# Kernel tuning notes

Measured on AMD Instinct MI355X. Metric: run time of the kernel, lower is better.

The kernel has to match this reference:

```python
import jax, jax.numpy as jnp
import numpy as np

NUM_EXPERTS = 64
TOP_K = 8
LOAD_EMA_DECAY = 0.999
BIAS_TEMPERATURE = 1.0
NOISE_STD = 0.01


def setup_inputs() -> dict:
    key = jax.random.key(0)
    k1, k2, k3, k4 = jax.random.split(key, 4)
    hidden_states = jax.random.normal(k1, (4, 4096, 2048), dtype=jnp.float32)
    router_w = jax.random.normal(k2, (NUM_EXPERTS, 2048), dtype=jnp.float32) * 0.02
    expert_loads = jax.random.uniform(k3, (NUM_EXPERTS,), dtype=jnp.float32)
    bias_strength = jnp.ones((1,), dtype=jnp.float32)
    noise = jax.random.normal(k4, (4 * 4096, NUM_EXPERTS), dtype=jnp.float32)
    return {
        "hidden_states": hidden_states,
        "router_w": router_w,
        "expert_loads": expert_loads,
        "bias_strength": bias_strength,
        "noise": noise,
    }


def reference(hidden_states, router_w, expert_loads, bias_strength, noise):
    # Training-mode forward with total_routed > 0 (adaptive bias active),
    # balance_loss_weight = 0 (aux_loss is None in the original).
    E = NUM_EXPERTS
    x = hidden_states.reshape(-1, hidden_states.shape[-1])  # [N, d]
    n_tokens = x.shape[0]

    # Router linear (no bias) + training noise
    logits = jnp.einsum("nd,ed->ne", x, router_w) + noise * NOISE_STD  # [N, E]

    # Adaptive load-based bias (core of aux-loss-free routing)
    q = expert_loads / jnp.clip(expert_loads.sum(), 1e-8)  # normalized loads
    t = 1.0 / E  # expected uniform load
    # F.kl_div(log q, t, reduction='sum') = sum_e t*(log t - log q_e)
    kl = jnp.sum(t * (jnp.log(t) - jnp.log(jnp.clip(q, 1e-8))))
    adaptive_strength = jax.nn.sigmoid(kl * 10.0)
    new_bias_strength = 0.9 * bias_strength[0] + 0.1 * adaptive_strength
    bias = jnp.tanh((q - t) * E) * BIAS_TEMPERATURE * new_bias_strength  # [E]
    logits = logits - bias[None, :]

    # Top-k selection + softmax gating over selected logits
    expert_weights, expert_indices = jax.lax.top_k(logits, TOP_K)  # [N, K]
    expert_weights = jax.nn.softmax(expert_weights, axis=-1)

    # EMA load-statistics update (scatter-add of gate weights per expert)
    batch_loads = jax.ops.segment_sum(
        expert_weights.reshape(-1), expert_indices.reshape(-1), num_segments=E
    ) / n_tokens
    new_expert_loads = LOAD_EMA_DECAY * expert_loads + (1.0 - LOAD_EMA_DECAY) * batch_loads

    return expert_indices, expert_weights, new_expert_loads, new_bias_strength
```

## Files before the change

### kernel.cpp

```cpp
#include <hip/hip_runtime.h>
#include <hip/hip_bf16.h>
#include <math.h>

#define NT 16384
#define DIM 2048
#define NE 64
#define TK 8

typedef _Float16 f16_t;
typedef _Float16 half8 __attribute__((ext_vector_type(8)));
typedef float floatx16 __attribute__((ext_vector_type(16)));

__global__ __launch_bounds__(256) void prep_kernel(const float* __restrict__ w,
                                                   const float* __restrict__ expert_loads,
                                                   const float* __restrict__ bias_strength,
                                                   float* __restrict__ ws_bias,
                                                   float* __restrict__ ws_batch,
                                                   f16_t* __restrict__ whi,
                                                   f16_t* __restrict__ wlo,
                                                   float* __restrict__ out_bias_strength) {
    if (blockIdx.x == 64) {
        int e = threadIdx.x;
        if (e < 64) {
            float load = expert_loads[e];
            float s = load;
            #pragma unroll
            for (int off = 32; off >= 1; off >>= 1) s += __shfl_xor(s, off, 64);
            s = fmaxf(s, 1e-8f);
            float q = load / s;
            const float t = 1.0f / 64.0f;
            float kl = t * (logf(t) - logf(fmaxf(q, 1e-8f)));
            #pragma unroll
            for (int off = 32; off >= 1; off >>= 1) kl += __shfl_xor(kl, off, 64);
            float as = 1.0f / (1.0f + expf(-10.0f * kl));
            float nbs = 0.9f * bias_strength[0] + 0.1f * as;
            ws_bias[e] = tanhf((q - t) * 64.0f) * nbs;
            ws_batch[e] = 0.0f;
            if (e == 0) out_bias_strength[0] = nbs;
        }
        return;
    }
    int idx = blockIdx.x * 256 + threadIdx.x;
    int lane = idx & 63;
    int tile = (idx >> 6) & 1;
    int c    = idx >> 7;
    int n = tile * 32 + (lane & 31);
    int k = c * 16 + (lane >> 5) * 8;
    const float* src = w + (size_t)n * DIM + k;
    float4 a = *(const float4*)src;
    float4 b = *(const float4*)(src + 4);
    float v[8] = {a.x, a.y, a.z, a.w, b.x, b.y, b.z, b.w};
    half8 h, l;
    #pragma unroll
    for (int j = 0; j < 8; ++j) {
        f16_t hh = (f16_t)v[j];
        h[j] = hh;
        l[j] = (f16_t)(v[j] - (float)hh);
    }
    *(half8*)(whi + (size_t)idx * 8) = h;
    *(half8*)(wlo + (size_t)idx * 8) = l;
}

__global__ __launch_bounds__(256) void router_main(const float* __restrict__ x,
                                                   const f16_t* __restrict__ whi,
                                                   const f16_t* __restrict__ wlo,
                                                   const float* __restrict__ noise,
                                                   const float* __restrict__ ws_bias,
                                                   float* __restrict__ ws_batch,
                                                   float* __restrict__ out) {
    __shared__ float part[4][32][72];
    __shared__ float bias_sh[64];
    __shared__ float loads_sh[64];

    const int tid = threadIdx.x;
    const int wv  = tid >> 6;
    const int L   = tid & 63;
    const int r   = L & 31;
    const int kh  = L >> 5;
    const int token0 = blockIdx.x * 32;

    if (tid < 64) { bias_sh[tid] = ws_bias[tid]; loads_sh[tid] = 0.0f; }

    const float* xp = x + (size_t)(token0 + r) * DIM + wv * 512 + kh * 8;
    const half8* whi8 = (const half8*)whi;
    const half8* wlo8 = (const half8*)wlo;

    floatx16 acc0, acc1;
    #pragma unroll
    for (int i = 0; i < 16; ++i) { acc0[i] = 0.0f; acc1[i] = 0.0f; }

    #pragma unroll 4
    for (int c = 0; c < 32; ++c) {
        float4 a0 = *(const float4*)(xp + c * 16);
        float4 a1 = *(const float4*)(xp + c * 16 + 4);
        int base = ((wv * 32 + c) * 2) * 64 + L;
        half8 b0h = whi8[base];
        half8 b1h = whi8[base + 64];
        half8 b0l = wlo8[base];
        half8 b1l = wlo8[base + 64];
        float xv[8] = {a0.x, a0.y, a0.z, a0.w, a1.x, a1.y, a1.z, a1.w};
        half8 ah, al;
        #pragma unroll
        for (int j = 0; j < 8; ++j) {
            f16_t h = (f16_t)xv[j];
            ah[j] = h;
            al[j] = (f16_t)(xv[j] - (float)h);
        }
        acc0 = __builtin_amdgcn_mfma_f32_32x32x16_f16(ah, b0h, acc0, 0, 0, 0);
        acc1 = __builtin_amdgcn_mfma_f32_32x32x16_f16(ah, b1h, acc1, 0, 0, 0);
        acc0 = __builtin_amdgcn_mfma_f32_32x32x16_f16(al, b0h, acc0, 0, 0, 0);
        acc1 = __builtin_amdgcn_mfma_f32_32x32x16_f16(al, b1h, acc1, 0, 0, 0);
        acc0 = __builtin_amdgcn_mfma_f32_32x32x16_f16(ah, b0l, acc0, 0, 0, 0);
        acc1 = __builtin_amdgcn_mfma_f32_32x32x16_f16(ah, b1l, acc1, 0, 0, 0);
    }

    #pragma unroll
    for (int reg = 0; reg < 16; ++reg) {
        int row = (reg & 3) + 8 * (reg >> 2) + 4 * kh;
        part[wv][row][r]      = acc0[reg];
        part[wv][row][32 + r] = acc1[reg];
    }
    __syncthreads();

    #pragma unroll
    for (int p = 0; p < 8; ++p) {
        int o = tid + p * 256;
        int t = o >> 6, e = o & 63;
        float s = part[0][t][e] + part[1][t][e] + part[2][t][e] + part[3][t][e];
        s += noise[(size_t)(token0 + t) * NE + e] * 0.01f - bias_sh[e];
        part[0][t][e] = s;
    }
    __syncthreads();

    if (tid < 32) {
        int t = tid;
        float tv[TK]; int ti_[TK];
        #pragma unroll
        for (int j = 0; j < TK; ++j) { tv[j] = -INFINITY; ti_[j] = 0; }
        for (int e = 0; e < NE; ++e) {
            float v = part[0][t][e]; int id = e;
            #pragma unroll
            for (int j = 0; j < TK; ++j) {
                bool gt = v > tv[j];
                float nv = gt ? v : tv[j];
                int   ni = gt ? id : ti_[j];
                float ov = gt ? tv[j] : v;
                int   oi = gt ? ti_[j] : id;
                tv[j] = nv; ti_[j] = ni; v = ov; id = oi;
            }
        }
        float m = tv[0], ssum = 0.0f, wvv[TK];
        #pragma unroll
        for (int j = 0; j < TK; ++j) { wvv[j] = expf(tv[j] - m); ssum += wvv[j]; }
        float inv = 1.0f / ssum;
        size_t gt_ = (size_t)(token0 + t);
        #pragma unroll
        for (int j = 0; j < TK; ++j) {
            float wgt = wvv[j] * inv;
            out[gt_ * TK + j] = (float)ti_[j];
            out[(size_t)NT * TK + gt_ * TK + j] = wgt;
            atomicAdd(&loads_sh[ti_[j]], wgt);
        }
    }
    __syncthreads();
    if (tid < 64) atomicAdd(&ws_batch[tid], loads_sh[tid]);
}

__global__ __launch_bounds__(64) void finalize_kernel(const float* __restrict__ expert_loads,
                                                      const float* __restrict__ ws_batch,
                                                      float* __restrict__ out_loads) {
    int e = threadIdx.x;
    out_loads[e] = 0.999f * expert_loads[e] + 0.001f * (ws_batch[e] / (float)NT);
}

extern "C" void kernel_launch(void* const* d_in, const int* in_sizes, int n_in,
                              void* d_out, int out_size, void* d_ws, size_t ws_size,
                              hipStream_t stream) {
    const float* x     = (const float*)d_in[0];
    const float* rw    = (const float*)d_in[1];
    const float* loads = (const float*)d_in[2];
    const float* bs    = (const float*)d_in[3];
    const float* noise = (const float*)d_in[4];
    float* out = (float*)d_out;
    float* ws  = (float*)d_ws;
    float* ws_bias  = ws;
    float* ws_batch = ws + 64;
    f16_t* whi = (f16_t*)(ws + 128);
    f16_t* wlo = whi + (size_t)16384 * 8;

    prep_kernel<<<65, 256, 0, stream>>>(rw, loads, bs, ws_bias, ws_batch, whi, wlo,
                                        out + (size_t)NT * TK * 2 + NE);
    router_main<<<NT / 32, 256, 0, stream>>>(x, whi, wlo, noise, ws_bias, ws_batch, out);
    finalize_kernel<<<1, 64, 0, stream>>>(loads, ws_batch, out + (size_t)NT * TK * 2);
}
```

Baseline: 222.0 us.

## Stage activations through LDS via async global_load_lds and split K across eight waves

The router GEMM now loads x tiles straight into LDS with global_load_lds, as coalesced row segments, and then reads MFMA fragments back from LDS. Before, each lane did strided float4 loads from global memory. The block grows to 512 threads, so eight waves each handle 256 of the K dimension, and the cross-wave reduction now sums eight partials. The aim is better global coalescing and more waves in flight on this memory-bound kernel. The cost is extra LDS traffic, per-chunk waits that block without double buffering, and a larger shared footprint that may limit occupancy.

```diff
diff --git a/kernel.cpp b/kernel.cpp
--- a/kernel.cpp
+++ b/kernel.cpp
@@ -10,6 +10,9 @@
 typedef _Float16 f16_t;
 typedef _Float16 half8 __attribute__((ext_vector_type(8)));
 typedef float floatx16 __attribute__((ext_vector_type(16)));
+
+typedef __attribute__((address_space(3))) unsigned int  lds_u32;
+typedef __attribute__((address_space(1))) const unsigned int gbl_u32;
 
 __global__ __launch_bounds__(256) void prep_kernel(const float* __restrict__ w,
                                                    const float* __restrict__ expert_loads,
@@ -61,14 +64,14 @@
     *(half8*)(wlo + (size_t)idx * 8) = l;
 }
 
-__global__ __launch_bounds__(256) void router_main(const float* __restrict__ x,
-                                                   const f16_t* __restrict__ whi,
-                                                   const f16_t* __restrict__ wlo,
-                                                   const float* __restrict__ noise,
-                                                   const float* __restrict__ ws_bias,
-                                                   float* __restrict__ ws_batch,
-                                                   float* __restrict__ out) {
-    __shared__ float part[4][32][72];
+__global__ __launch_bounds__(512, 4) void router_main(const float* __restrict__ x,
+                                                      const f16_t* __restrict__ whi,
+                                                      const f16_t* __restrict__ wlo,
+                                                      const float* __restrict__ noise,
+                                                      const float* __restrict__ ws_bias,
+                                                      float* __restrict__ ws_batch,
+                                                      float* __restrict__ out) {
+    __shared__ float smem[17408];
     __shared__ float bias_sh[64];
     __shared__ float loads_sh[64];
 
@@ -81,7 +84,7 @@
 
     if (tid < 64) { bias_sh[tid] = ws_bias[tid]; loads_sh[tid] = 0.0f; }
 
-    const float* xp = x + (size_t)(token0 + r) * DIM + wv * 512 + kh * 8;
+    char* mybuf = (char*)smem + wv * 8320;
     const half8* whi8 = (const half8*)whi;
     const half8* wlo8 = (const half8*)wlo;
 
@@ -89,46 +92,69 @@
     #pragma unroll
     for (int i = 0; i < 16; ++i) { acc0[i] = 0.0f; acc1[i] = 0.0f; }
 
-    #pragma unroll 4
-    for (int c = 0; c < 32; ++c) {
-        float4 a0 = *(const float4*)(xp + c * 16);
-        float4 a1 = *(const float4*)(xp + c * 16 + 4);
-        int base = ((wv * 32 + c) * 2) * 64 + L;
-        half8 b0h = whi8[base];
-        half8 b1h = whi8[base + 64];
-        half8 b0l = wlo8[base];
-        half8 b1l = wlo8[base + 64];
-        float xv[8] = {a0.x, a0.y, a0.z, a0.w, a1.x, a1.y, a1.z, a1.w};
-        half8 ah, al;
-        #pragma unroll
-        for (int j = 0; j < 8; ++j) {
-            f16_t h = (f16_t)xv[j];
-            ah[j] = h;
-            al[j] = (f16_t)(xv[j] - (float)h);
-        }
-        acc0 = __builtin_amdgcn_mfma_f32_32x32x16_f16(ah, b0h, acc0, 0, 0, 0);
-        acc1 = __builtin_amdgcn_mfma_f32_32x32x16_f16(ah, b1h, acc1, 0, 0, 0);
-        acc0 = __builtin_amdgcn_mfma_f32_32x32x16_f16(al, b0h, acc0, 0, 0, 0);
-        acc1 = __builtin_amdgcn_mfma_f32_32x32x16_f16(al, b1h, acc1, 0, 0, 0);
-        acc0 = __builtin_amdgcn_mfma_f32_32x32x16_f16(ah, b0l, acc0, 0, 0, 0);
-        acc1 = __builtin_amdgcn_mfma_f32_32x32x16_f16(ah, b1l, acc1, 0, 0, 0);
-    }
+    const int srow = L >> 4;
+    const int sb   = (L & 15) * 16;
+    const float* xbase = x + (size_t)token0 * DIM + wv * 256;
+
+    const int gfrag = r >> 2;
+    const int mfrag = r & 3;
+
+    for (int ch = 0; ch < 4; ++ch) {
+        asm volatile("s_waitcnt lgkmcnt(0)" ::: "memory");
+        #pragma unroll
+        for (int g = 0; g < 8; ++g) {
+            const char* gp = (const char*)(xbase + (size_t)(4 * g + srow) * DIM + ch * 64) + sb;
+            __builtin_amdgcn_global_load_lds((gbl_u32*)gp, (lds_u32*)(mybuf + g * 1040), 16, 0, 0);
+        }
+        asm volatile("s_waitcnt vmcnt(0)" ::: "memory");
+
+        #pragma unroll
+        for (int cc = 0; cc < 4; ++cc) {
+            const int c16 = wv * 16 + ch * 4 + cc;
+            const float* fp = (const float*)(mybuf + gfrag * 1040 + mfrag * 256 + cc * 64 + kh * 32);
+            float4 a0 = *(const float4*)fp;
+            float4 a1 = *(const float4*)(fp + 4);
+            float xv[8] = {a0.x, a0.y, a0.z, a0.w, a1.x, a1.y, a1.z, a1.w};
+            half8 ah, al;
+            #pragma unroll
+            for (int j = 0; j < 8; ++j) {
+                f16_t h = (f16_t)xv[j];
+                ah[j] = h;
+                al[j] = (f16_t)(xv[j] - (float)h);
+            }
+            const int bidx = (c16 * 2) * 64 + L;
+            half8 b0h = whi8[bidx];
+            half8 b1h = whi8[bidx + 64];
+            half8 b0l = wlo8[bidx];
+            half8 b1l = wlo8[bidx + 64];
+            acc0 = __builtin_amdgcn_mfma_f32_32x32x16_f16(ah, b0h, acc0, 0, 0, 0);
+            acc1 = __builtin_amdgcn_mfma_f32_32x32x16_f16(ah, b1h, acc1, 0, 0, 0);
+            acc0 = __builtin_amdgcn_mfma_f32_32x32x16_f16(al, b0h, acc0, 0, 0, 0);
+            acc1 = __builtin_amdgcn_mfma_f32_32x32x16_f16(al, b1h, acc1, 0, 0, 0);
+            acc0 = __builtin_amdgcn_mfma_f32_32x32x16_f16(ah, b0l, acc0, 0, 0, 0);
+            acc1 = __builtin_amdgcn_mfma_f32_32x32x16_f16(ah, b1l, acc1, 0, 0, 0);
+        }
+    }
+
+    __syncthreads();
 
     #pragma unroll
     for (int reg = 0; reg < 16; ++reg) {
         int row = (reg & 3) + 8 * (reg >> 2) + 4 * kh;
-        part[wv][row][r]      = acc0[reg];
-        part[wv][row][32 + r] = acc1[reg];
-    }
-    __syncthreads();
-
-    #pragma unroll
-    for (int p = 0; p < 8; ++p) {
-        int o = tid + p * 256;
+        smem[wv * 2176 + row * 68 + r]      = acc0[reg];
+        smem[wv * 2176 + row * 68 + 32 + r] = acc1[reg];
+    }
+    __syncthreads();
+
+    #pragma unroll
+    for (int p = 0; p < 4; ++p) {
+        int o = tid + p * 512;
         int t = o >> 6, e = o & 63;
-        float s = part[0][t][e] + part[1][t][e] + part[2][t][e] + part[3][t][e];
+        float s = 0.0f;
+        #pragma unroll
+        for (int q = 0; q < 8; ++q) s += smem[q * 2176 + t * 68 + e];
         s += noise[(size_t)(token0 + t) * NE + e] * 0.01f - bias_sh[e];
-        part[0][t][e] = s;
+        smem[t * 68 + e] = s;
     }
     __syncthreads();
 
@@ -138,7 +164,7 @@
         #pragma unroll
         for (int j = 0; j < TK; ++j) { tv[j] = -INFINITY; ti_[j] = 0; }
         for (int e = 0; e < NE; ++e) {
-            float v = part[0][t][e]; int id = e;
+            float v = smem[t * 68 + e]; int id = e;
             #pragma unroll
             for (int j = 0; j < TK; ++j) {
                 bool gt = v > tv[j];
@@ -190,6 +216,6 @@
 
     prep_kernel<<<65, 256, 0, stream>>>(rw, loads, bs, ws_bias, ws_batch, whi, wlo,
                                         out + (size_t)NT * TK * 2 + NE);
-    router_main<<<NT / 32, 256, 0, stream>>>(x, whi, wlo, noise, ws_bias, ws_batch, out);
+    router_main<<<NT / 32, 512, 0, stream>>>(x, whi, wlo, noise, ws_bias, ws_batch, out);
     finalize_kernel<<<1, 64, 0, stream>>>(loads, ws_batch, out + (size_t)NT * TK * 2);
 }
```

After: 221.4 us. About the same (-0.3%).
